# Performance work log

Measured on AMD Instinct MI355X. Metric: run time of the kernel, lower is better.

## Reference

```python
import jax, jax.numpy as jnp
import numpy as np

EPS = 1e-5
P = 3  # p_size
BW = 1.0  # bandwidth


def _instance_norm(x):
    # calc_mean_std: per (B,C) mean/std over spatial dims, unbiased var (torch default)
    b, c, h, w = x.shape
    flat = x.reshape(b, c, h * w)
    mean = flat.mean(-1)[:, :, None, None]
    std = jnp.sqrt(flat.var(-1, ddof=1) + EPS)[:, :, None, None]
    return (x - mean) / std


def _conv1x1(x, w, bias):
    # x: (B,C,H,W), w: (O,C), bias: (O,)
    return jnp.einsum('oc,bchw->bohw', w, x) + bias[None, :, None, None]


def _patches_scaled(x, scale):
    # ReflectionPad2d(1) + Unfold(3) -> (B, HW, C*9), torch layout (c slow, k fast),
    # with ContextAtten scale applied over the 9 kernel positions.
    b, c, h, w = x.shape
    pad = jnp.pad(x, ((0, 0), (0, 0), (1, 1), (1, 1)), mode='reflect')
    # (B,C,H,W,9)
    p9 = jnp.stack([pad[:, :, di:di + h, dj:dj + w]
                    for di in range(P) for dj in range(P)], axis=-1)
    p9 = p9 * scale  # broadcast over last (kernel) axis
    # -> (B,H,W,C,9) -> (B, HW, C*9)
    return p9.transpose(0, 2, 3, 1, 4).reshape(b, h * w, c * P * P)


def setup_inputs() -> dict:
    key = jax.random.key(0)
    ks = jax.random.split(key, 12)
    B, C, H, W = 2, 512, 64, 64
    IC = 256
    f32 = jnp.float32
    inp = {
        'content': jax.random.normal(ks[0], (B, C, H, W), f32),
        'style': jax.random.normal(ks[1], (B, C, H, W), f32),
        'fusion_style': jax.random.normal(ks[2], (B, C, H, W), f32),
        'theta_w': jax.random.normal(ks[3], (IC, C), f32) * np.sqrt(2.0 / C),
        'theta_b': jnp.zeros((IC,), f32),
        'phi_w': jax.random.normal(ks[4], (IC, C), f32) * np.sqrt(2.0 / C),
        'phi_b': jnp.zeros((IC,), f32),
        'g_w': jax.random.normal(ks[5], (IC, C), f32) * np.sqrt(2.0 / C),
        'g_b': jnp.zeros((IC,), f32),
        'W_w': jax.random.normal(ks[6], (C, IC), f32) * np.sqrt(2.0 / IC),
        'W_b': jnp.zeros((C,), f32),
        'scale': jnp.ones((P * P,), f32),
    }
    return inp


def reference(content, style, fusion_style, theta_w, theta_b, phi_w, phi_b,
              g_w, g_b, W_w, W_b, scale):
    B, C, H, W = content.shape
    IC = theta_w.shape[0]
    HW = H * W

    # g on fusion_style -> (B, HW, IC)
    g_s = _conv1x1(fusion_style, g_w, g_b).reshape(B, IC, HW).transpose(0, 2, 1)

    # instance-normalize content/style (normal=True path)
    xn = _instance_norm(content)
    sn = _instance_norm(style)

    theta_x = _conv1x1(xn, theta_w, theta_b)
    phi_s = _conv1x1(sn, phi_w, phi_b)

    theta_p = _patches_scaled(theta_x, scale)  # (B, HW, IC*9)
    phi_p = _patches_scaled(phi_s, scale)      # (B, HW, IC*9)

    f = jnp.einsum('blk,bmk->blm', theta_p, phi_p) * BW  # (B, HW, HW)
    f_div_C = jax.nn.softmax(f, axis=-1)

    y = jnp.einsum('blm,bmo->blo', f_div_C, g_s)  # (B, HW, IC)
    y = y.transpose(0, 2, 1).reshape(B, IC, H, W)
    W_y = _conv1x1(y, W_w, W_b)  # (B, C, H, W)
    # isTraining=True path: conf_map = 0
    return W_y
```

## Files before the change

kernel.cpp:

```cpp
#include <hip/hip_runtime.h>
#include <stdint.h>

typedef __attribute__((ext_vector_type(8))) __bf16 bf16x8;
typedef __attribute__((ext_vector_type(4))) float f32x4;
typedef __attribute__((ext_vector_type(4))) unsigned int uint4v;

__device__ __forceinline__ float bf2f(unsigned short u){
  unsigned int x = ((unsigned int)u) << 16;
  return __builtin_bit_cast(float, x);
}
__device__ __forceinline__ unsigned short f2bf(float f){
  unsigned int x = __builtin_bit_cast(unsigned int, f);
  x += 0x7FFFu + ((x >> 16) & 1u);
  return (unsigned short)(x >> 16);
}

#define OUT_PART 4
#define OUT_PARTH 5

template<int OM>
__global__ __launch_bounds__(256)
void gemm_bt(const unsigned short* __restrict__ A, int lda,
             const unsigned short* __restrict__ Bt, int ldb,
             int kchunk, void* __restrict__ Out, int ldo,
             size_t zStride, size_t aBatch, size_t bBatch,
             int sMask, int sShift)
{
  __shared__ uint4v AsmBuf[1024];
  __shared__ uint4v BsmBuf[1024];
  char* Asm = (char*)AsmBuf;
  char* Bsm = (char*)BsmBuf;

  const int tid  = threadIdx.x;
  const int lane = tid & 63;
  const int wave = tid >> 6;
  const int wy = wave >> 1, wx = wave & 1;
  const int lm = lane & 15, quad = lane >> 4;
  const int tileM = blockIdx.y * 128;
  const int tileN = blockIdx.x * 128;
  const int z = blockIdx.z;
  const int slice = z & sMask;
  const int batch = z >> sShift;

  A  += (size_t)slice*kchunk + (size_t)batch*aBatch;
  Bt += (size_t)slice*kchunk + (size_t)batch*bBatch;

  const int sr0 = tid >> 2, sc0 = tid & 3;
  const int sr1 = sr0 + 64;
  const size_t gA0 = (size_t)(tileM + sr0)*lda + ((sc0 ^ ((sr0 >> 1) & 3)) << 3);
  const size_t gA1 = (size_t)(tileM + sr1)*lda + ((sc0 ^ ((sr1 >> 1) & 3)) << 3);
  const size_t gB0 = (size_t)(tileN + sr0)*ldb + ((sc0 ^ ((sr0 >> 1) & 3)) << 3);
  const size_t gB1 = (size_t)(tileN + sr1)*ldb + ((sc0 ^ ((sr1 >> 1) & 3)) << 3);
  const int lOff0 = sr0*64 + sc0*16;
  const int lOff1 = sr1*64 + sc0*16;

  int aOff[4], bOff[4];
#pragma unroll
  for (int t = 0; t < 4; ++t){
    int ra = wy*64 + t*16 + lm;
    aOff[t] = ra*64 + ((quad ^ ((ra >> 1) & 3)) << 4);
    int rb = wx*64 + t*16 + lm;
    bOff[t] = rb*64 + ((quad ^ ((rb >> 1) & 3)) << 4);
  }

  f32x4 acc[4][4] = {};

  const int ksteps = kchunk >> 5;
  uint4v a0v = *(const uint4v*)(A + gA0);
  uint4v a1v = *(const uint4v*)(A + gA1);
  uint4v b0v = *(const uint4v*)(Bt + gB0);
  uint4v b1v = *(const uint4v*)(Bt + gB1);

  for (int kt = 0; kt < ksteps; ++kt){
    char* As = Asm + (kt & 1)*8192;
    char* Bs = Bsm + (kt & 1)*8192;
    *(uint4v*)(As + lOff0) = a0v;
    *(uint4v*)(As + lOff1) = a1v;
    *(uint4v*)(Bs + lOff0) = b0v;
    *(uint4v*)(Bs + lOff1) = b1v;
    __syncthreads();
    if (kt + 1 < ksteps){
      const unsigned short* Ak = A + (kt + 1)*32;
      const unsigned short* Bk = Bt + (kt + 1)*32;
      a0v = *(const uint4v*)(Ak + gA0);
      a1v = *(const uint4v*)(Ak + gA1);
      b0v = *(const uint4v*)(Bk + gB0);
      b1v = *(const uint4v*)(Bk + gB1);
    }
    bf16x8 af[4], bfr[4];
#pragma unroll
    for (int t = 0; t < 4; ++t){
      af[t]  = __builtin_bit_cast(bf16x8, *(const uint4v*)(As + aOff[t]));
      bfr[t] = __builtin_bit_cast(bf16x8, *(const uint4v*)(Bs + bOff[t]));
    }
#pragma unroll
    for (int tm = 0; tm < 4; ++tm)
#pragma unroll
      for (int tn = 0; tn < 4; ++tn)
        acc[tm][tn] = __builtin_amdgcn_mfma_f32_16x16x32_bf16(af[tm], bfr[tn], acc[tm][tn], 0, 0, 0);
  }

#pragma unroll
  for (int tm = 0; tm < 4; ++tm){
    const int rowb = tileM + wy*64 + tm*16 + quad*4;
#pragma unroll
    for (int tn = 0; tn < 4; ++tn){
      const int col = tileN + wx*64 + tn*16 + lm;
#pragma unroll
      for (int r = 0; r < 4; ++r){
        const float v = acc[tm][tn][r];
        const size_t idx = (size_t)z*zStride + (size_t)(rowb + r)*ldo + col;
        if (OM == OUT_PART) ((float*)Out)[idx] = v;
        else                ((unsigned short*)Out)[idx] = f2bf(v);
      }
    }
  }
}

__global__ __launch_bounds__(256)
void gemm_big(const unsigned short* __restrict__ A, int lda,
              const unsigned short* __restrict__ Bt, int ldb,
              int K, float* __restrict__ Out, int ldo,
              size_t aBatch, size_t bBatch, size_t oBatch)
{
  __shared__ uint4v AsmBuf[2048];
  __shared__ uint4v BsmBuf[1024];
  char* Asm = (char*)AsmBuf;
  char* Bsm = (char*)BsmBuf;

  const int tid  = threadIdx.x;
  const int lane = tid & 63;
  const int wave = tid >> 6;
  const int wy = wave >> 1, wx = wave & 1;
  const int lm = lane & 15, quad = lane >> 4;
  const int tileM = blockIdx.y * 256;
  const int tileN = blockIdx.x * 128;
  const int z = blockIdx.z;

  A  += (size_t)z*aBatch;
  Bt += (size_t)z*bBatch;
  Out += (size_t)z*oBatch;

  const int sr = tid >> 2, sc = tid & 3;
  size_t gA[4]; int lA[4];
  size_t gB[2]; int lB[2];
#pragma unroll
  for (int i = 0; i < 4; ++i){
    const int r = sr + 64*i;
    gA[i] = (size_t)(tileM + r)*lda + ((sc ^ ((r >> 1) & 3)) << 3);
    lA[i] = r*64 + sc*16;
  }
#pragma unroll
  for (int i = 0; i < 2; ++i){
    const int r = sr + 64*i;
    gB[i] = (size_t)(tileN + r)*ldb + ((sc ^ ((r >> 1) & 3)) << 3);
    lB[i] = r*64 + sc*16;
  }

  int aOff[8], bOff[4];
#pragma unroll
  for (int t = 0; t < 8; ++t){
    const int ra = wy*128 + t*16 + lm;
    aOff[t] = ra*64 + ((quad ^ ((ra >> 1) & 3)) << 4);
  }
#pragma unroll
  for (int t = 0; t < 4; ++t){
    const int rb = wx*64 + t*16 + lm;
    bOff[t] = rb*64 + ((quad ^ ((rb >> 1) & 3)) << 4);
  }

  f32x4 acc[8][4] = {};

  const int ksteps = K >> 5;
  uint4v av[4], bv[2];
#pragma unroll
  for (int i = 0; i < 4; ++i) av[i] = *(const uint4v*)(A + gA[i]);
#pragma unroll
  for (int i = 0; i < 2; ++i) bv[i] = *(const uint4v*)(Bt + gB[i]);

  for (int kt = 0; kt < ksteps; ++kt){
    char* As = Asm + (kt & 1)*16384;
    char* Bs = Bsm + (kt & 1)*8192;
#pragma unroll
    for (int i = 0; i < 4; ++i) *(uint4v*)(As + lA[i]) = av[i];
#pragma unroll
    for (int i = 0; i < 2; ++i) *(uint4v*)(Bs + lB[i]) = bv[i];
    __syncthreads();
    if (kt + 1 < ksteps){
      const unsigned short* Ak = A + (kt + 1)*32;
      const unsigned short* Bk = Bt + (kt + 1)*32;
#pragma unroll
      for (int i = 0; i < 4; ++i) av[i] = *(const uint4v*)(Ak + gA[i]);
#pragma unroll
      for (int i = 0; i < 2; ++i) bv[i] = *(const uint4v*)(Bk + gB[i]);
    }
    bf16x8 af[8], bfr[4];
#pragma unroll
    for (int t = 0; t < 8; ++t)
      af[t] = __builtin_bit_cast(bf16x8, *(const uint4v*)(As + aOff[t]));
#pragma unroll
    for (int t = 0; t < 4; ++t)
      bfr[t] = __builtin_bit_cast(bf16x8, *(const uint4v*)(Bs + bOff[t]));
#pragma unroll
    for (int tm = 0; tm < 8; ++tm)
#pragma unroll
      for (int tn = 0; tn < 4; ++tn)
        acc[tm][tn] = __builtin_amdgcn_mfma_f32_16x16x32_bf16(af[tm], bfr[tn], acc[tm][tn], 0, 0, 0);
  }

#pragma unroll
  for (int tm = 0; tm < 8; ++tm){
    const int rowb = tileM + wy*128 + tm*16 + quad*4;
#pragma unroll
    for (int tn = 0; tn < 4; ++tn){
      const int col = tileN + wx*64 + tn*16 + lm;
#pragma unroll
      for (int r = 0; r < 4; ++r)
        Out[(size_t)(rowb + r)*ldo + col] = acc[tm][tn][r];
    }
  }
}

__global__ __launch_bounds__(256)
void reduce_tp(const float* __restrict__ part,
               const float* __restrict__ tb, const float* __restrict__ pb,
               unsigned short* __restrict__ th, unsigned short* __restrict__ ph)
{
  const size_t i = (size_t)blockIdx.x*256 + threadIdx.x;
  const int which = (int)(i >> 21);
  const size_t j = i & 0x1FFFFFu;
  const int col = (int)(j & 255u);
  float v = 0.f;
#pragma unroll
  for (int s = 0; s < 4; ++s)
    v += part[(size_t)((which << 2) + s)*2097152 + j];
  v += (which ? pb : tb)[col];
  unsigned short hi = f2bf(v);
  unsigned short lo = f2bf(v - bf2f(hi));
  const size_t o = (j >> 8)*768 + col;
  unsigned short* O = which ? ph : th;
  const int dup = which ? 512 : 256;
  const int loo = which ? 256 : 512;
  O[o] = hi; O[o + dup] = hi; O[o + loo] = lo;
}

__global__ __launch_bounds__(256)
void reduce_g(const unsigned short* __restrict__ part,
              const float* __restrict__ gb, unsigned short* __restrict__ gs)
{
  const size_t i = (size_t)blockIdx.x*256 + threadIdx.x;
  float v = 0.f;
#pragma unroll
  for (int s = 0; s < 4; ++s) v += bf2f(part[(size_t)s*2097152 + i]);
  gs[i] = f2bf(v + gb[i >> 13]);
}

__global__ __launch_bounds__(256)
void reduce_y(const unsigned short* __restrict__ part,
              unsigned short* __restrict__ yb)
{
  const size_t i = (size_t)blockIdx.x*256 + threadIdx.x;
  const int b = (int)(i >> 20);
  const size_t j = i & 0xFFFFFu;
  float v = 0.f;
#pragma unroll
  for (int s = 0; s < 8; ++s)
    v += bf2f(part[(size_t)((b << 3) + s)*1048576 + j]);
  yb[i] = f2bf(v);
}

__global__ __launch_bounds__(256)
void reduce_w(const float* __restrict__ part, const float* __restrict__ wb,
              void* __restrict__ Out, const unsigned int* __restrict__ flagPtr)
{
  const size_t i = (size_t)blockIdx.x*256 + threadIdx.x;
  const int b = (int)(i >> 21);
  const size_t j = i & 0x1FFFFFu;
  float v = part[(size_t)(b << 1)*2097152 + j]
          + part[(size_t)((b << 1) | 1)*2097152 + j]
          + wb[(i >> 12) & 511u];
  if (flagPtr[0]) ((float*)Out)[i] = v;
  else            ((unsigned short*)Out)[i] = f2bf(v);
}

__global__ __launch_bounds__(256)
void detect_prep(const void* __restrict__ content,
                 const void* tb, const void* pb, const void* gb, const void* wb,
                 const void* sc,
                 unsigned int* __restrict__ flag, float* __restrict__ scale_c,
                 float* tb_c, float* pb_c, float* gb_c, float* wb_c)
{
  __shared__ int cnt;
  __shared__ unsigned int flg;
  const int tid = threadIdx.x;
  if (tid == 0) cnt = 0;
  __syncthreads();
  unsigned int w = ((const unsigned int*)content)[tid];
  int e = (w >> 23) & 0xFF;
  if (e >= 0x70 && e <= 0x8F) atomicAdd(&cnt, 1);
  __syncthreads();
  if (tid == 0){ flg = (cnt >= 128) ? 1u : 0u; flag[0] = flg; }
  __syncthreads();
  const unsigned int f = flg;
  auto rd = [&](const void* p, int i)->float{
    return f ? ((const float*)p)[i] : bf2f(((const unsigned short*)p)[i]);
  };
  if (tid < 9) scale_c[tid] = rd(sc, tid);
  tb_c[tid] = rd(tb, tid);
  pb_c[tid] = rd(pb, tid);
  gb_c[tid] = rd(gb, tid);
  wb_c[tid] = rd(wb, tid);
  wb_c[tid + 256] = rd(wb, tid + 256);
}

__global__ __launch_bounds__(256)
void conv_weights(const void* tw, const void* pw, const void* gw, const void* www,
                  const unsigned int* __restrict__ flagPtr,
                  unsigned short* __restrict__ wdup,
                  unsigned short* __restrict__ gwc,
                  unsigned short* __restrict__ wwc)
{
  const unsigned int fl = flagPtr[0];
  const int sec = blockIdx.y;
  const int idx = blockIdx.x*256 + threadIdx.x;
  auto rd = [&](const void* p, int i)->float{
    return fl ? ((const float*)p)[i] : bf2f(((const unsigned short*)p)[i]);
  };
  if (sec < 2){
    const void* w = sec ? pw : tw;
    const int o = idx >> 9, c = idx & 511;
    float v = rd(w, o*512 + c);
    unsigned short hi = f2bf(v);
    unsigned short lo = f2bf(v - bf2f(hi));
    unsigned short* base = wdup + (size_t)sec*256*1536 + o*1536;
    base[c] = hi; base[512 + c] = lo; base[1024 + c] = hi;
  } else if (sec == 2){
    const int o = idx >> 9, c = idx & 511;
    gwc[o*512 + c] = f2bf(rd(gw, o*512 + c));
  } else {
    const int o = idx >> 8, c = idx & 255;
    wwc[o*256 + c] = f2bf(rd(www, o*256 + c));
  }
}

__global__ __launch_bounds__(256)
void stats_all(const void* __restrict__ content, const void* __restrict__ style,
               const unsigned int* __restrict__ flagPtr,
               float* __restrict__ statsC, float* __restrict__ statsS)
{
  const unsigned int fl = flagPtr[0];
  const void* X = blockIdx.z ? style : content;
  float* stats = blockIdx.z ? statsS : statsC;
  const int bc = blockIdx.x;
  const int tid = threadIdx.x;
  float s = 0.f, q = 0.f;
  if (fl){
    const f32x4* row = (const f32x4*)((const float*)X + (size_t)bc*4096);
#pragma unroll
    for (int i = 0; i < 4; ++i){
      f32x4 v = row[tid + i*256];
#pragma unroll
      for (int j = 0; j < 4; ++j){ s += v[j]; q += v[j]*v[j]; }
    }
  } else {
    const uint4v* row = (const uint4v*)((const unsigned short*)X + (size_t)bc*4096);
#pragma unroll
    for (int i = 0; i < 2; ++i){
      uint4v u = row[tid + i*256];
#pragma unroll
      for (int j = 0; j < 4; ++j){
        float a = bf2f((unsigned short)(u[j] & 0xffffu));
        float b = bf2f((unsigned short)(u[j] >> 16));
        s += a + b; q += a*a + b*b;
      }
    }
  }
#pragma unroll
  for (int off = 32; off > 0; off >>= 1){
    s += __shfl_down(s, off);
    q += __shfl_down(q, off);
  }
  __shared__ float rs[4], rq[4];
  if ((tid & 63) == 0){ rs[tid >> 6] = s; rq[tid >> 6] = q; }
  __syncthreads();
  if (tid == 0){
    s = rs[0] + rs[1] + rs[2] + rs[3];
    q = rq[0] + rq[1] + rq[2] + rq[3];
    float mean = s * (1.0f/4096.0f);
    float var  = (q - 4096.0f*mean*mean) * (1.0f/4095.0f);
    stats[bc*2 + 0] = mean;
    stats[bc*2 + 1] = 1.0f / sqrtf(var + 1e-5f);
  }
}

__global__ __launch_bounds__(256)
void norm_all(const void* __restrict__ content, const void* __restrict__ style,
              const void* __restrict__ fusion,
              const float* __restrict__ statsC, const float* __restrict__ statsS,
              unsigned short* __restrict__ xn, unsigned short* __restrict__ sn,
              unsigned short* __restrict__ fst,
              const unsigned int* __restrict__ flagPtr)
{
  __shared__ float tile[64][65];
  const unsigned int fl = flagPtr[0];
  const int z = blockIdx.z;
  const int which = z >> 1;
  const int b  = z & 1;
  const int l0 = blockIdx.x * 64;
  const int c0 = blockIdx.y * 64;
  const int tid = threadIdx.x;
  const int tx = tid & 63, ty = tid >> 6;

  const void* X = which == 0 ? content : (which == 1 ? style : fusion);
#pragma unroll
  for (int p = 0; p < 16; ++p){
    const int cc = ty + p*4;
    const size_t src = ((size_t)b*512 + c0 + cc)*4096 + l0 + tx;
    tile[cc][tx] = fl ? ((const float*)X)[src]
                      : bf2f(((const unsigned short*)X)[src]);
  }
  __syncthreads();
  if (which < 2){
    const float* stats = which ? statsS : statsC;
    const float mean = stats[(b*512 + c0 + tx)*2 + 0];
    const float inv  = stats[(b*512 + c0 + tx)*2 + 1];
    unsigned short* Out = which ? sn : xn;
#pragma unroll
    for (int p = 0; p < 16; ++p){
      const int lj = ty + p*4;
      const float v = (tile[tx][lj] - mean) * inv;
      const size_t o = ((size_t)b*4096 + l0 + lj)*1536 + c0 + tx;
      const unsigned short hi = f2bf(v);
      Out[o] = hi;
      Out[o + 512] = hi;
      Out[o + 1024] = f2bf(v - bf2f(hi));
    }
  } else {
#pragma unroll
    for (int p = 0; p < 16; ++p){
      const int lj = ty + p*4;
      const size_t o = ((size_t)b*4096 + l0 + lj)*512 + c0 + tx;
      fst[o] = f2bf(tile[tx][lj]);
    }
  }
}

__global__ __launch_bounds__(256)
void softmax_rows(const float* __restrict__ Gbase, const float* __restrict__ scale_c,
                  unsigned short* __restrict__ Pbase)
{
  const int bb = blockIdx.x >> 12;
  const int l  = blockIdx.x & 4095;
  const float* G = Gbase + (size_t)bb*16777216;
  unsigned short* P = Pbase + (size_t)bb*16777216;
  const int yy = l >> 6, xx = l & 63;
  const int tid = threadIdx.x;

  float s2[9];
  const float* rowp[9];
#pragma unroll
  for (int di = 0; di < 3; ++di){
    int ry = yy + di - 1; ry = ry < 0 ? 1 : (ry > 63 ? 62 : ry);
#pragma unroll
    for (int dj = 0; dj < 3; ++dj){
      int rx = xx + dj - 1; rx = rx < 0 ? 1 : (rx > 63 ? 62 : rx);
      const int k = di*3 + dj;
      const float s = scale_c[k];
      s2[k] = s*s;
      rowp[k] = G + (size_t)(ry*64 + rx)*4096;
    }
  }

  float fv[16];
  float mx = -3.0e38f;
#pragma unroll
  for (int i = 0; i < 16; ++i){
    const int m = tid + i*256;
    const int my = m >> 6, mxo = m & 63;
    int cy[3], cx[3];
#pragma unroll
    for (int d = 0; d < 3; ++d){
      int t0 = my + d - 1;  cy[d] = (t0 < 0 ? 1 : (t0 > 63 ? 62 : t0))*64;
      int t1 = mxo + d - 1; cx[d] = (t1 < 0 ? 1 : (t1 > 63 ? 62 : t1));
    }
    float v = 0.f;
#pragma unroll
    for (int di = 0; di < 3; ++di)
#pragma unroll
      for (int dj = 0; dj < 3; ++dj)
        v = fmaf(s2[di*3+dj], rowp[di*3+dj][cy[di] + cx[dj]], v);
    fv[i] = v;
    mx = fmaxf(mx, v);
  }

  __shared__ float redA[4], redB[4];
#pragma unroll
  for (int off = 32; off > 0; off >>= 1) mx = fmaxf(mx, __shfl_down(mx, off));
  if ((tid & 63) == 0) redA[tid >> 6] = mx;
  __syncthreads();
  mx = fmaxf(fmaxf(redA[0], redA[1]), fmaxf(redA[2], redA[3]));

  float sum = 0.f;
#pragma unroll
  for (int i = 0; i < 16; ++i){ fv[i] = __expf(fv[i] - mx); sum += fv[i]; }
#pragma unroll
  for (int off = 32; off > 0; off >>= 1) sum += __shfl_down(sum, off);
  if ((tid & 63) == 0) redB[tid >> 6] = sum;
  __syncthreads();
  sum = redB[0] + redB[1] + redB[2] + redB[3];
  const float inv = 1.0f / sum;

  unsigned short* Prow = P + (size_t)l*4096;
#pragma unroll
  for (int i = 0; i < 16; ++i) Prow[tid + i*256] = f2bf(fv[i]*inv);
}

extern "C" void kernel_launch(void* const* d_in, const int* in_sizes, int n_in,
                              void* d_out, int out_size, void* d_ws, size_t ws_size,
                              hipStream_t stream)
{
  const void* content = d_in[0];
  const void* style   = d_in[1];
  const void* fusion  = d_in[2];
  const void* theta_w = d_in[3];
  const void* theta_b = d_in[4];
  const void* phi_w   = d_in[5];
  const void* phi_b   = d_in[6];
  const void* g_w     = d_in[7];
  const void* g_b     = d_in[8];
  const void* W_w     = d_in[9];
  const void* W_b     = d_in[10];
  const void* scale   = d_in[11];

  char* ws = (char*)d_ws;
  size_t off = 0;
  auto take = [&](size_t bytes)->char*{
    char* p = ws + off; off += (bytes + 255) & ~(size_t)255; return p;
  };

  unsigned int* flag  = (unsigned int*)take(256);
  float* scale_c      = (float*)take(256);
  float* tb_c         = (float*)take(1024);
  float* pb_c         = (float*)take(1024);
  float* gb_c         = (float*)take(1024);
  float* wb_c         = (float*)take(2048);
  float* statsC       = (float*)take(1024ull*2*4);
  float* statsS       = (float*)take(1024ull*2*4);
  unsigned short* wdup = (unsigned short*)take(2ull*256*1536*2);
  unsigned short* gwc  = (unsigned short*)take(256ull*512*2);
  unsigned short* wwc  = (unsigned short*)take(512ull*256*2);
  unsigned short* th   = (unsigned short*)take(8192ull*768*2);
  unsigned short* ph   = (unsigned short*)take(8192ull*768*2);
  unsigned short* gs   = (unsigned short*)take(256ull*8192*2);
  unsigned short* yb   = (unsigned short*)take(2ull*4096*256*2);
  float* G0            = (float*)take(4096ull*4096*4);
  float* G1            = (float*)take(4096ull*4096*4);
  char* unionC         = take(64ull*1024*1024);
  unsigned short* xn   = (unsigned short*)unionC;
  unsigned short* sn   = (unsigned short*)(unionC + 8192ull*1536*2);
  unsigned short* fst  = (unsigned short*)(unionC + 2ull*8192*1536*2);
  unsigned short* P    = (unsigned short*)unionC;

  float* partTP          = G0;
  unsigned short* partG  = (unsigned short*)G1;
  unsigned short* partY  = (unsigned short*)G0;
  float* partW           = G1;

  detect_prep<<<1, 256, 0, stream>>>(content, theta_b, phi_b, g_b, W_b, scale,
                                     flag, scale_c, tb_c, pb_c, gb_c, wb_c);
  conv_weights<<<dim3(512,4), 256, 0, stream>>>(theta_w, phi_w, g_w, W_w, flag,
                                                wdup, gwc, wwc);
  stats_all<<<dim3(1024,1,2), 256, 0, stream>>>(content, style, flag, statsC, statsS);
  norm_all<<<dim3(64,8,6), 256, 0, stream>>>(content, style, fusion,
                                             statsC, statsS, xn, sn, fst, flag);

  gemm_bt<OUT_PART><<<dim3(2,64,8), 256, 0, stream>>>(
      xn, 1536, wdup, 1536, 384, partTP, 256, 8192ull*256,
      8192ull*1536, 256ull*1536, 3, 2);
  reduce_tp<<<16384, 256, 0, stream>>>(partTP, tb_c, pb_c, th, ph);

  gemm_bt<OUT_PARTH><<<dim3(64,2,4), 256, 0, stream>>>(
      gwc, 512, fst, 512, 128, partG, 8192, 256ull*8192, 0, 0, 3, 2);
  reduce_g<<<8192, 256, 0, stream>>>(partG, gb_c, gs);

  gemm_big<<<dim3(32,16,2), 256, 0, stream>>>(
      th, 768, ph, 768, 768, G0, 4096,
      4096ull*768, 4096ull*768, (size_t)(G1 - G0));

  softmax_rows<<<8192, 256, 0, stream>>>(G0, scale_c, P);

  gemm_bt<OUT_PARTH><<<dim3(2,32,16), 256, 0, stream>>>(
      P, 4096, gs, 8192, 512, partY, 256, 4096ull*256,
      16777216ull, 4096ull, 7, 3);
  reduce_y<<<8192, 256, 0, stream>>>(partY, yb);

  gemm_bt<OUT_PART><<<dim3(32,4,4), 256, 0, stream>>>(
      wwc, 256, yb, 256, 128, partW, 4096, 512ull*4096,
      0, 4096ull*256, 1, 1);
  reduce_w<<<16384, 256, 0, stream>>>(partW, wb_c, d_out, flag);
}
```

Measured before the change: 394.5 us.

## Add 128x256 wide GEMM tile and load gemm_big B fragments directly from global

Adds a gemm_wide kernel with a 128x256 tile and uses it for the theta/phi projection and the P·g GEMM, so one block covers the full N=256 width and reads each A row once instead of twice. In gemm_big, the B operand no longer goes through LDS: each lane loads its MFMA fragments straight from global memory into registers, prefetched one k-step ahead. This cuts LDS traffic and shared memory use. The cost is more registers per thread, fewer blocks for the projection GEMMs, and uncoalesced 16-byte strided global reads for B.

```diff
diff --git a/kernel.cpp b/kernel.cpp
--- a/kernel.cpp
+++ b/kernel.cpp
@@ -117,6 +117,117 @@
   }
 }
 
+template<int OM>
+__global__ __launch_bounds__(256)
+void gemm_wide(const unsigned short* __restrict__ A, int lda,
+               const unsigned short* __restrict__ Bt, int ldb,
+               int kchunk, void* __restrict__ Out, int ldo,
+               size_t zStride, size_t aBatch, size_t bBatch,
+               int sMask, int sShift)
+{
+  __shared__ uint4v AsmBuf[1024];
+  __shared__ uint4v BsmBuf[2048];
+  char* Asm = (char*)AsmBuf;
+  char* Bsm = (char*)BsmBuf;
+
+  const int tid  = threadIdx.x;
+  const int lane = tid & 63;
+  const int wave = tid >> 6;
+  const int wy = wave >> 1, wx = wave & 1;
+  const int lm = lane & 15, quad = lane >> 4;
+  const int tileM = blockIdx.y * 128;
+  const int tileN = blockIdx.x * 256;
+  const int z = blockIdx.z;
+  const int slice = z & sMask;
+  const int batch = z >> sShift;
+
+  A  += (size_t)slice*kchunk + (size_t)batch*aBatch;
+  Bt += (size_t)slice*kchunk + (size_t)batch*bBatch;
+
+  const int sr = tid >> 2, sc = tid & 3;
+  size_t gA[2]; int lA[2];
+  size_t gB[4]; int lB[4];
+#pragma unroll
+  for (int i = 0; i < 2; ++i){
+    const int r = sr + 64*i;
+    gA[i] = (size_t)(tileM + r)*lda + ((sc ^ ((r >> 1) & 3)) << 3);
+    lA[i] = r*64 + sc*16;
+  }
+#pragma unroll
+  for (int i = 0; i < 4; ++i){
+    const int r = sr + 64*i;
+    gB[i] = (size_t)(tileN + r)*ldb + ((sc ^ ((r >> 1) & 3)) << 3);
+    lB[i] = r*64 + sc*16;
+  }
+
+  int aOff[4], bOff[8];
+#pragma unroll
+  for (int t = 0; t < 4; ++t){
+    const int ra = wy*64 + t*16 + lm;
+    aOff[t] = ra*64 + ((quad ^ ((ra >> 1) & 3)) << 4);
+  }
+#pragma unroll
+  for (int t = 0; t < 8; ++t){
+    const int rb = wx*128 + t*16 + lm;
+    bOff[t] = rb*64 + ((quad ^ ((rb >> 1) & 3)) << 4);
+  }
+
+  f32x4 acc[4][8] = {};
+
+  const int ksteps = kchunk >> 5;
+  uint4v av[2], bv[4];
+#pragma unroll
+  for (int i = 0; i < 2; ++i) av[i] = *(const uint4v*)(A + gA[i]);
+#pragma unroll
+  for (int i = 0; i < 4; ++i) bv[i] = *(const uint4v*)(Bt + gB[i]);
+
+  for (int kt = 0; kt < ksteps; ++kt){
+    char* As = Asm + (kt & 1)*8192;
+    char* Bs = Bsm + (kt & 1)*16384;
+#pragma unroll
+    for (int i = 0; i < 2; ++i) *(uint4v*)(As + lA[i]) = av[i];
+#pragma unroll
+    for (int i = 0; i < 4; ++i) *(uint4v*)(Bs + lB[i]) = bv[i];
+    __syncthreads();
+    if (kt + 1 < ksteps){
+      const unsigned short* Ak = A + (kt + 1)*32;
+      const unsigned short* Bk = Bt + (kt + 1)*32;
+#pragma unroll
+      for (int i = 0; i < 2; ++i) av[i] = *(const uint4v*)(Ak + gA[i]);
+#pragma unroll
+      for (int i = 0; i < 4; ++i) bv[i] = *(const uint4v*)(Bk + gB[i]);
+    }
+    bf16x8 af[4], bfr[8];
+#pragma unroll
+    for (int t = 0; t < 4; ++t)
+      af[t] = __builtin_bit_cast(bf16x8, *(const uint4v*)(As + aOff[t]));
+#pragma unroll
+    for (int t = 0; t < 8; ++t)
+      bfr[t] = __builtin_bit_cast(bf16x8, *(const uint4v*)(Bs + bOff[t]));
+#pragma unroll
+    for (int tm = 0; tm < 4; ++tm)
+#pragma unroll
+      for (int tn = 0; tn < 8; ++tn)
+        acc[tm][tn] = __builtin_amdgcn_mfma_f32_16x16x32_bf16(af[tm], bfr[tn], acc[tm][tn], 0, 0, 0);
+  }
+
+#pragma unroll
+  for (int tm = 0; tm < 4; ++tm){
+    const int rowb = tileM + wy*64 + tm*16 + quad*4;
+#pragma unroll
+    for (int tn = 0; tn < 8; ++tn){
+      const int col = tileN + wx*128 + tn*16 + lm;
+#pragma unroll
+      for (int r = 0; r < 4; ++r){
+        const float v = acc[tm][tn][r];
+        const size_t idx = (size_t)z*zStride + (size_t)(rowb + r)*ldo + col;
+        if (OM == OUT_PART) ((float*)Out)[idx] = v;
+        else                ((unsigned short*)Out)[idx] = f2bf(v);
+      }
+    }
+  }
+}
+
 __global__ __launch_bounds__(256)
 void gemm_big(const unsigned short* __restrict__ A, int lda,
               const unsigned short* __restrict__ Bt, int ldb,
@@ -124,9 +235,7 @@
               size_t aBatch, size_t bBatch, size_t oBatch)
 {
   __shared__ uint4v AsmBuf[2048];
-  __shared__ uint4v BsmBuf[1024];
   char* Asm = (char*)AsmBuf;
-  char* Bsm = (char*)BsmBuf;
 
   const int tid  = threadIdx.x;
   const int lane = tid & 63;
@@ -143,69 +252,63 @@
 
   const int sr = tid >> 2, sc = tid & 3;
   size_t gA[4]; int lA[4];
-  size_t gB[2]; int lB[2];
 #pragma unroll
   for (int i = 0; i < 4; ++i){
     const int r = sr + 64*i;
     gA[i] = (size_t)(tileM + r)*lda + ((sc ^ ((r >> 1) & 3)) << 3);
     lA[i] = r*64 + sc*16;
   }
-#pragma unroll
-  for (int i = 0; i < 2; ++i){
-    const int r = sr + 64*i;
-    gB[i] = (size_t)(tileN + r)*ldb + ((sc ^ ((r >> 1) & 3)) << 3);
-    lB[i] = r*64 + sc*16;
-  }
-
-  int aOff[8], bOff[4];
+
+  int aOff[8];
 #pragma unroll
   for (int t = 0; t < 8; ++t){
     const int ra = wy*128 + t*16 + lm;
     aOff[t] = ra*64 + ((quad ^ ((ra >> 1) & 3)) << 4);
   }
+  size_t gBF[4];
 #pragma unroll
   for (int t = 0; t < 4; ++t){
     const int rb = wx*64 + t*16 + lm;
-    bOff[t] = rb*64 + ((quad ^ ((rb >> 1) & 3)) << 4);
+    gBF[t] = (size_t)(tileN + rb)*ldb + quad*8;
   }
 
   f32x4 acc[8][4] = {};
 
   const int ksteps = K >> 5;
-  uint4v av[4], bv[2];
+  uint4v av[4];
 #pragma unroll
   for (int i = 0; i < 4; ++i) av[i] = *(const uint4v*)(A + gA[i]);
-#pragma unroll
-  for (int i = 0; i < 2; ++i) bv[i] = *(const uint4v*)(Bt + gB[i]);
+  bf16x8 bnx[4];
+#pragma unroll
+  for (int t = 0; t < 4; ++t)
+    bnx[t] = __builtin_bit_cast(bf16x8, *(const uint4v*)(Bt + gBF[t]));
 
   for (int kt = 0; kt < ksteps; ++kt){
     char* As = Asm + (kt & 1)*16384;
-    char* Bs = Bsm + (kt & 1)*8192;
 #pragma unroll
     for (int i = 0; i < 4; ++i) *(uint4v*)(As + lA[i]) = av[i];
-#pragma unroll
-    for (int i = 0; i < 2; ++i) *(uint4v*)(Bs + lB[i]) = bv[i];
     __syncthreads();
+    bf16x8 bcur[4];
+#pragma unroll
+    for (int t = 0; t < 4; ++t) bcur[t] = bnx[t];
     if (kt + 1 < ksteps){
       const unsigned short* Ak = A + (kt + 1)*32;
       const unsigned short* Bk = Bt + (kt + 1)*32;
 #pragma unroll
       for (int i = 0; i < 4; ++i) av[i] = *(const uint4v*)(Ak + gA[i]);
 #pragma unroll
-      for (int i = 0; i < 2; ++i) bv[i] = *(const uint4v*)(Bk + gB[i]);
-    }
-    bf16x8 af[8], bfr[4];
+      for (int t = 0; t < 4; ++t)
+        bnx[t] = __builtin_bit_cast(bf16x8, *(const uint4v*)(Bk + gBF[t]));
+    }
+    bf16x8 af[8];
 #pragma unroll
     for (int t = 0; t < 8; ++t)
       af[t] = __builtin_bit_cast(bf16x8, *(const uint4v*)(As + aOff[t]));
 #pragma unroll
-    for (int t = 0; t < 4; ++t)
-      bfr[t] = __builtin_bit_cast(bf16x8, *(const uint4v*)(Bs + bOff[t]));
-#pragma unroll
     for (int tm = 0; tm < 8; ++tm)
 #pragma unroll
       for (int tn = 0; tn < 4; ++tn)
-        acc[tm][tn] = __builtin_amdgcn_mfma_f32_16x16x32_bf16(af[tm], bfr[tn], acc[tm][tn], 0, 0, 0);
+        acc[tm][tn] = __builtin_amdgcn_mfma_f32_16x16x32_bf16(af[tm], bcur[tn], acc[tm][tn], 0, 0, 0);
   }
 
 #pragma unroll
@@ -574,7 +677,7 @@
   norm_all<<<dim3(64,8,6), 256, 0, stream>>>(content, style, fusion,
                                              statsC, statsS, xn, sn, fst, flag);
 
-  gemm_bt<OUT_PART><<<dim3(2,64,8), 256, 0, stream>>>(
+  gemm_wide<OUT_PART><<<dim3(1,64,8), 256, 0, stream>>>(
       xn, 1536, wdup, 1536, 384, partTP, 256, 8192ull*256,
       8192ull*1536, 256ull*1536, 3, 2);
   reduce_tp<<<16384, 256, 0, stream>>>(partTP, tb_c, pb_c, th, ph);
@@ -589,7 +692,7 @@
 
   softmax_rows<<<8192, 256, 0, stream>>>(G0, scale_c, P);
 
-  gemm_bt<OUT_PARTH><<<dim3(2,32,16), 256, 0, stream>>>(
+  gemm_wide<OUT_PARTH><<<dim3(1,32,16), 256, 0, stream>>>(
       P, 4096, gs, 8192, 512, partY, 256, 4096ull*256,
       16777216ull, 4096ull, 7, 3);
   reduce_y<<<8192, 256, 0, stream>>>(partY, yb);
```

After: 394.4 us. No clear change (-0.0%).
